# Performance work log

Hardware: AMD Instinct MI355X
Metric: run time of the kernel (lower is better)

Reference implementation:

```python
import jax, jax.numpy as jnp
import numpy as np
import math

N_HEADS = 16


def setup_inputs() -> dict:
    key = jax.random.key(0)
    ks = jax.random.split(key, 8)
    B, N, H = 4, 1024, 1024
    hidden_states = jax.random.normal(ks[0], (B, N, H), dtype=jnp.float32)
    # per-sample valid length in [N//2, N]; padding_vector is nonzero on valid
    # positions, zero afterwards (first zero index defines the pad boundary)
    lengths = jax.random.randint(ks[1], (B,), N // 2, N + 1)
    padding_vector = (jnp.arange(N)[None, :] < lengths[:, None]).astype(jnp.int32)
    s = 0.02
    Wq = jax.random.normal(ks[2], (H, H), dtype=jnp.float32) * s
    Wk = jax.random.normal(ks[3], (H, H), dtype=jnp.float32) * s
    Wv = jax.random.normal(ks[4], (H, H), dtype=jnp.float32) * s
    bq = jnp.zeros((H,), dtype=jnp.float32)
    bk = jnp.zeros((H,), dtype=jnp.float32)
    bv = jnp.zeros((H,), dtype=jnp.float32)
    return dict(hidden_states=hidden_states, padding_vector=padding_vector,
                Wq=Wq, bq=bq, Wk=Wk, bk=bk, Wv=Wv, bv=bv, max_n_codes=N)


def _heads(x, n_heads):
    B, N, H = x.shape
    return x.reshape(B, N, n_heads, H // n_heads).transpose(0, 2, 1, 3)  # (B,h,N,d)


def reference(hidden_states, padding_vector, Wq, bq, Wk, bk, Wv, bv, max_n_codes):
    B, N, H = hidden_states.shape
    d = H // N_HEADS
    q = _heads(hidden_states @ Wq.T + bq, N_HEADS)  # (B,h,N,d)
    k = _heads(hidden_states @ Wk.T + bk, N_HEADS)
    v = _heads(hidden_states @ Wv.T + bv, N_HEADS)
    scores = jnp.einsum('bhnd,bhmd->bhnm', q, k) / math.sqrt(d)
    # padd = index of first zero in padding_vector, or N if no zero
    is_zero = padding_vector == 0
    padd = jnp.where(is_zero.any(axis=1), jnp.argmax(is_zero, axis=1), N)  # (B,)
    idx = jnp.arange(N)
    valid = idx[None, :] < padd[:, None]                      # (B,N)
    keep = valid[:, None, :, None] & valid[:, None, None, :]  # (B,1,N,N)
    # masked positions get -inf pre-softmax, then are zeroed post-softmax.
    # finfo.min instead of -inf keeps fully-masked rows NaN-free; they are
    # zeroed by the post-softmax mask exactly as in the torch version.
    neg = jnp.finfo(scores.dtype).min
    probs = jax.nn.softmax(jnp.where(keep, scores, neg), axis=-1)
    probs = jnp.where(keep, probs, 0.0)
    attention_values = probs.sum(axis=-2)                     # (B,h,N)
    context = jnp.einsum('bhnm,bhmd->bhnd', probs, v)
    return (attention_values, k, q, context, scores)
```

## Files before the change

kernel.cpp:

```cpp
#include <hip/hip_runtime.h>
#include <math.h>

#define B_ 4
#define N_ 1024
#define H_ 1024
#define NH_ 16
#define D_ 64

#define SZ_ATTN (B_*NH_*N_)
#define SZ_HEADS (B_*NH_*N_*D_)

typedef __attribute__((ext_vector_type(8))) short short8v;
typedef __attribute__((ext_vector_type(4))) short short4v;
typedef __attribute__((ext_vector_type(4))) float floatx4;

__device__ inline unsigned short f2bf(float x) {
    union { float f; unsigned int u; } v; v.f = x;
    unsigned int r = v.u + 0x7FFFu + ((v.u >> 16) & 1u);
    return (unsigned short)(r >> 16);
}
__device__ inline float bf2f(unsigned short u) {
    union { unsigned int i; float f; } v; v.i = ((unsigned int)u) << 16;
    return v.f;
}

__global__ void padd_kernel(const int* __restrict__ pv, int* __restrict__ padd) {
    __shared__ int mn;
    const int b = blockIdx.x;
    if (threadIdx.x == 0) mn = N_;
    __syncthreads();
    for (int m = threadIdx.x; m < N_; m += blockDim.x)
        if (pv[b*N_ + m] == 0) atomicMin(&mn, m);
    __syncthreads();
    if (threadIdx.x == 0) padd[b] = mn;
}

__global__ __launch_bounds__(256)
void proj3_mfma_kernel(const float* __restrict__ X,
                       const float* __restrict__ Wq, const float* __restrict__ bq_, float* __restrict__ Oq,
                       const float* __restrict__ Wk, const float* __restrict__ bk_, float* __restrict__ Ok,
                       const float* __restrict__ Wv, const float* __restrict__ bv_, float* __restrict__ Ov)
{
    const int which = blockIdx.z;
    const float* __restrict__ W    = (which == 0) ? Wq  : (which == 1) ? Wk  : Wv;
    const float* __restrict__ bias = (which == 0) ? bq_ : (which == 1) ? bk_ : bv_;
    float* __restrict__ outH       = (which == 0) ? Oq  : (which == 1) ? Ok  : Ov;

    __shared__ __align__(16) unsigned short Abf[128*64];
    __shared__ __align__(16) unsigned short Bbf[128*64];

    const int tid  = threadIdx.x;
    const int lane = tid & 63;
    const int w    = tid >> 6;
    const int wr   = w >> 1, wc = w & 1;
    const int fr   = lane & 15, hi = lane >> 4;
    const int i0 = blockIdx.y * 128;
    const int j0 = blockIdx.x * 128;

    floatx4 acc[4][4];
    #pragma unroll
    for (int mi = 0; mi < 4; ++mi)
        #pragma unroll
        for (int ni = 0; ni < 4; ++ni)
            acc[mi][ni] = (floatx4){0.f, 0.f, 0.f, 0.f};

    for (int kt = 0; kt < H_; kt += 64) {
        __syncthreads();
        #pragma unroll
        for (int l = 0; l < 4; ++l) {
            const int e = tid + 256*l;
            const int row = e >> 3, kc = e & 7;
            const int sw = ((kc ^ (row & 7)) << 3);
            {
                const float* src = X + (size_t)(i0+row)*H_ + kt + kc*8;
                const float4 xa = *(const float4*)(src);
                const float4 xb = *(const float4*)(src + 4);
                short8v pk;
                pk[0] = (short)f2bf(xa.x); pk[1] = (short)f2bf(xa.y);
                pk[2] = (short)f2bf(xa.z); pk[3] = (short)f2bf(xa.w);
                pk[4] = (short)f2bf(xb.x); pk[5] = (short)f2bf(xb.y);
                pk[6] = (short)f2bf(xb.z); pk[7] = (short)f2bf(xb.w);
                *(short8v*)&Abf[row*64 + sw] = pk;
            }
            {
                const float* src = W + (size_t)(j0+row)*H_ + kt + kc*8;
                const float4 wa = *(const float4*)(src);
                const float4 wb = *(const float4*)(src + 4);
                short8v pk;
                pk[0] = (short)f2bf(wa.x); pk[1] = (short)f2bf(wa.y);
                pk[2] = (short)f2bf(wa.z); pk[3] = (short)f2bf(wa.w);
                pk[4] = (short)f2bf(wb.x); pk[5] = (short)f2bf(wb.y);
                pk[6] = (short)f2bf(wb.z); pk[7] = (short)f2bf(wb.w);
                *(short8v*)&Bbf[row*64 + sw] = pk;
            }
        }
        __syncthreads();

        #pragma unroll
        for (int ks = 0; ks < 2; ++ks) {
            short8v a[4], b[4];
            #pragma unroll
            for (int mi = 0; mi < 4; ++mi) {
                const int row = wr*64 + mi*16 + fr;
                a[mi] = *(const short8v*)&Abf[row*64 + (((ks*4 + hi) ^ (fr & 7)) << 3)];
            }
            #pragma unroll
            for (int ni = 0; ni < 4; ++ni) {
                const int row = wc*64 + ni*16 + fr;
                b[ni] = *(const short8v*)&Bbf[row*64 + (((ks*4 + hi) ^ (fr & 7)) << 3)];
            }
            #pragma unroll
            for (int mi = 0; mi < 4; ++mi)
                #pragma unroll
                for (int ni = 0; ni < 4; ++ni)
                    acc[mi][ni] = __builtin_amdgcn_mfma_f32_16x16x32_bf16(
                        a[mi], b[ni], acc[mi][ni], 0, 0, 0);
        }
    }

    #pragma unroll
    for (int ni = 0; ni < 4; ++ni) {
        const int j = j0 + wc*64 + ni*16 + fr;
        const int head = j >> 6, d = j & 63;
        const float bvj = bias[j];
        #pragma unroll
        for (int mi = 0; mi < 4; ++mi) {
            #pragma unroll
            for (int reg = 0; reg < 4; ++reg) {
                const int i = i0 + wr*64 + mi*16 + hi*4 + reg;
                const int bb = i >> 10, n = i & 1023;
                outH[((size_t)(bb*NH_ + head)*N_ + n)*D_ + d] = acc[mi][ni][reg] + bvj;
            }
        }
    }
}

__global__ __launch_bounds__(256)
void fused_attn_mfma(const float* __restrict__ Q, const float* __restrict__ K,
                     const float* __restrict__ Vh, const int* __restrict__ padd,
                     float* __restrict__ S, float* __restrict__ ctx,
                     float* __restrict__ attn)
{
    __shared__ __align__(16) unsigned short Abf[128*64];
    __shared__ __align__(16) unsigned short Bbf[64*64];
    __shared__ float smx[128], sinv[128];
    __shared__ float cred[256];

    const int tid  = threadIdx.x;
    const int lane = tid & 63;
    const int w    = tid >> 6;
    const int fr   = lane & 15, hi = lane >> 4;
    const int bh = blockIdx.y;
    const int n0 = blockIdx.x * 128;
    const int b  = bh >> 4;
    const int pd = padd[b];
    const float* Qb = Q  + (size_t)bh*N_*D_;
    const float* Kb = K  + (size_t)bh*N_*D_;
    const float* Vb = Vh + (size_t)bh*N_*D_;
    float* Sb = S + (size_t)bh*N_*N_;

    #pragma unroll
    for (int l = 0; l < 4; ++l) {
        const int e = tid + 256*l;
        const int row = e >> 3, kc = e & 7;
        const float* src = Qb + (size_t)(n0+row)*D_ + kc*8;
        const float4 xa = *(const float4*)(src);
        const float4 xb = *(const float4*)(src + 4);
        short8v pk;
        pk[0] = (short)f2bf(xa.x); pk[1] = (short)f2bf(xa.y);
        pk[2] = (short)f2bf(xa.z); pk[3] = (short)f2bf(xa.w);
        pk[4] = (short)f2bf(xb.x); pk[5] = (short)f2bf(xb.y);
        pk[6] = (short)f2bf(xb.z); pk[7] = (short)f2bf(xb.w);
        *(short8v*)&Abf[row*64 + ((kc ^ (row & 7)) << 3)] = pk;
    }
    __syncthreads();

    short8v qa[2][2];
    #pragma unroll
    for (int mi = 0; mi < 2; ++mi)
        #pragma unroll
        for (int ks = 0; ks < 2; ++ks) {
            const int arow = w*32 + mi*16 + fr;
            qa[mi][ks] = *(const short8v*)&Abf[arow*64 + (((ks*4 + hi) ^ (fr & 7)) << 3)];
        }

    float run_mx[2][4], run_sm[2][4];
    #pragma unroll
    for (int mi = 0; mi < 2; ++mi)
        #pragma unroll
        for (int reg = 0; reg < 4; ++reg) { run_mx[mi][reg] = -INFINITY; run_sm[mi][reg] = 0.f; }

    for (int m0 = 0; m0 < N_; m0 += 64) {
        #pragma unroll
        for (int l = 0; l < 2; ++l) {
            const int e = tid + 256*l;
            const int row = e >> 3, kc = e & 7;
            const float* src = Kb + (size_t)(m0+row)*D_ + kc*8;
            const float4 xa = *(const float4*)(src);
            const float4 xb = *(const float4*)(src + 4);
            short8v pk;
            pk[0] = (short)f2bf(xa.x); pk[1] = (short)f2bf(xa.y);
            pk[2] = (short)f2bf(xa.z); pk[3] = (short)f2bf(xa.w);
            pk[4] = (short)f2bf(xb.x); pk[5] = (short)f2bf(xb.y);
            pk[6] = (short)f2bf(xb.z); pk[7] = (short)f2bf(xb.w);
            *(short8v*)&Bbf[row*64 + ((kc ^ (row & 7)) << 3)] = pk;
        }
        __syncthreads();

        floatx4 sacc[2][4];
        #pragma unroll
        for (int mi = 0; mi < 2; ++mi)
            #pragma unroll
            for (int ni = 0; ni < 4; ++ni)
                sacc[mi][ni] = (floatx4){0.f, 0.f, 0.f, 0.f};

        #pragma unroll
        for (int ks = 0; ks < 2; ++ks) {
            short8v kb[4];
            #pragma unroll
            for (int ni = 0; ni < 4; ++ni) {
                const int brow = ni*16 + fr;
                kb[ni] = *(const short8v*)&Bbf[brow*64 + (((ks*4 + hi) ^ (fr & 7)) << 3)];
            }
            #pragma unroll
            for (int mi = 0; mi < 2; ++mi)
                #pragma unroll
                for (int ni = 0; ni < 4; ++ni)
                    sacc[mi][ni] = __builtin_amdgcn_mfma_f32_16x16x32_bf16(
                        qa[mi][ks], kb[ni], sacc[mi][ni], 0, 0, 0);
        }

        #pragma unroll
        for (int mi = 0; mi < 2; ++mi)
            #pragma unroll
            for (int ni = 0; ni < 4; ++ni) {
                sacc[mi][ni] *= 0.125f;
                const int m = m0 + ni*16 + fr;
                #pragma unroll
                for (int reg = 0; reg < 4; ++reg) {
                    const int n = n0 + w*32 + mi*16 + hi*4 + reg;
                    Sb[(size_t)n*N_ + m] = sacc[mi][ni][reg];
                }
            }

        if (m0 < pd) {
            #pragma unroll
            for (int mi = 0; mi < 2; ++mi)
                #pragma unroll
                for (int reg = 0; reg < 4; ++reg) {
                    float tm = -INFINITY;
                    #pragma unroll
                    for (int ni = 0; ni < 4; ++ni)
                        if (m0 + ni*16 + fr < pd) tm = fmaxf(tm, sacc[mi][ni][reg]);
                    tm = fmaxf(tm, __shfl_xor(tm, 1, 64));
                    tm = fmaxf(tm, __shfl_xor(tm, 2, 64));
                    tm = fmaxf(tm, __shfl_xor(tm, 4, 64));
                    tm = fmaxf(tm, __shfl_xor(tm, 8, 64));
                    const float nm = fmaxf(run_mx[mi][reg], tm);
                    float s = 0.f;
                    #pragma unroll
                    for (int ni = 0; ni < 4; ++ni)
                        if (m0 + ni*16 + fr < pd) s += __expf(sacc[mi][ni][reg] - nm);
                    s += __shfl_xor(s, 1, 64);
                    s += __shfl_xor(s, 2, 64);
                    s += __shfl_xor(s, 4, 64);
                    s += __shfl_xor(s, 8, 64);
                    run_sm[mi][reg] = run_sm[mi][reg]*__expf(run_mx[mi][reg] - nm) + s;
                    run_mx[mi][reg] = nm;
                }
        }
        __syncthreads();
    }

    if (n0 >= pd) {
        #pragma unroll
        for (int l = 0; l < 8; ++l) {
            const int e = tid + 256*l;
            const int row = e >> 4, c4 = e & 15;
            float4 z; z.x = z.y = z.z = z.w = 0.f;
            *(float4*)(ctx + ((size_t)bh*N_ + n0 + row)*D_ + c4*4) = z;
        }
        return;
    }

    if (fr == 0) {
        #pragma unroll
        for (int mi = 0; mi < 2; ++mi)
            #pragma unroll
            for (int reg = 0; reg < 4; ++reg) {
                const int row = w*32 + mi*16 + hi*4 + reg;
                const bool v = (n0 + row) < pd;
                smx[row]  = v ? run_mx[mi][reg] : 0.f;
                sinv[row] = v ? 1.f/run_sm[mi][reg] : 0.f;
            }
    }
    __syncthreads();

    floatx4 acc2[2][4];
    #pragma unroll
    for (int mi = 0; mi < 2; ++mi)
        #pragma unroll
        for (int ni = 0; ni < 4; ++ni)
            acc2[mi][ni] = (floatx4){0.f, 0.f, 0.f, 0.f};

    for (int m0 = 0; m0 < pd; m0 += 64) {
        #pragma unroll
        for (int l = 0; l < 8; ++l) {
            const int e = tid + 256*l;
            const int row = e >> 4, c4 = e & 15;
            const int n = n0 + row;
            const int m = m0 + c4*4;
            const float4 s4 = *(const float4*)(Sb + (size_t)n*N_ + m);
            const bool rv = n < pd;
            const float fmx = smx[row], fiv = sinv[row];
            short4v pk;
            pk[0] = (short)f2bf((rv && m+0 < pd) ? __expf(s4.x - fmx)*fiv : 0.f);
            pk[1] = (short)f2bf((rv && m+1 < pd) ? __expf(s4.y - fmx)*fiv : 0.f);
            pk[2] = (short)f2bf((rv && m+2 < pd) ? __expf(s4.z - fmx)*fiv : 0.f);
            pk[3] = (short)f2bf((rv && m+3 < pd) ? __expf(s4.w - fmx)*fiv : 0.f);
            const int elem = row*64 + (((c4 >> 1) ^ (row & 7)) << 3) + (c4 & 1)*4;
            *(short4v*)&Abf[elem] = pk;
        }
        {
            const int d = tid & 63, mg = tid >> 6;
            #pragma unroll
            for (int jj = 0; jj < 2; ++jj) {
                short8v pk;
                #pragma unroll
                for (int j = 0; j < 8; ++j)
                    pk[j] = (short)f2bf(Vb[(size_t)(m0 + mg*16 + jj*8 + j)*D_ + d]);
                const int chunk = mg*2 + jj;
                *(short8v*)&Bbf[d*64 + ((chunk ^ (d & 7)) << 3)] = pk;
            }
        }
        __syncthreads();

        {
            const int ml = tid & 63, q = tid >> 6;
            float cs = 0.f;
            #pragma unroll
            for (int i = 0; i < 32; ++i) {
                const int row = q*32 + i;
                cs += bf2f(Abf[row*64 + (((ml >> 3) ^ (row & 7)) << 3) + (ml & 7)]);
            }
            cred[tid] = cs;
        }
        __syncthreads();
        if (tid < 64) {
            const float vtot = cred[tid] + cred[tid+64] + cred[tid+128] + cred[tid+192];
            atomicAdd(&attn[(size_t)bh*N_ + m0 + tid], vtot);
        }

        #pragma unroll
        for (int ks = 0; ks < 2; ++ks) {
            short8v a[2], vfr[4];
            #pragma unroll
            for (int mi = 0; mi < 2; ++mi) {
                const int arow = w*32 + mi*16 + fr;
                a[mi] = *(const short8v*)&Abf[arow*64 + (((ks*4 + hi) ^ (fr & 7)) << 3)];
            }
            #pragma unroll
            for (int ni = 0; ni < 4; ++ni) {
                const int bd = ni*16 + fr;
                vfr[ni] = *(const short8v*)&Bbf[bd*64 + (((ks*4 + hi) ^ (fr & 7)) << 3)];
            }
            #pragma unroll
            for (int mi = 0; mi < 2; ++mi)
                #pragma unroll
                for (int ni = 0; ni < 4; ++ni)
                    acc2[mi][ni] = __builtin_amdgcn_mfma_f32_16x16x32_bf16(
                        a[mi], vfr[ni], acc2[mi][ni], 0, 0, 0);
        }
        __syncthreads();
    }

    #pragma unroll
    for (int mi = 0; mi < 2; ++mi)
        #pragma unroll
        for (int ni = 0; ni < 4; ++ni) {
            const int d = ni*16 + fr;
            #pragma unroll
            for (int reg = 0; reg < 4; ++reg) {
                const int n = n0 + w*32 + mi*16 + hi*4 + reg;
                ctx[((size_t)bh*N_ + n)*D_ + d] = acc2[mi][ni][reg];
            }
        }
}

extern "C" void kernel_launch(void* const* d_in, const int* in_sizes, int n_in,
                              void* d_out, int out_size, void* d_ws, size_t ws_size,
                              hipStream_t stream)
{
    const float* hs = (const float*)d_in[0];
    const int*   pv = (const int*)d_in[1];
    const float* Wq = (const float*)d_in[2];
    const float* bq = (const float*)d_in[3];
    const float* Wk = (const float*)d_in[4];
    const float* bk = (const float*)d_in[5];
    const float* Wv = (const float*)d_in[6];
    const float* bv = (const float*)d_in[7];
    float* out = (float*)d_out;

    float* out_attn = out;
    float* out_k    = out_attn + SZ_ATTN;
    float* out_q    = out_k + SZ_HEADS;
    float* out_ctx  = out_q + SZ_HEADS;
    float* out_sc   = out_ctx + SZ_HEADS;

    int*   padd = (int*)d_ws;
    float* v_ws = (float*)((char*)d_ws + 256);

    hipMemsetAsync(out_attn, 0, SZ_ATTN*sizeof(float), stream);
    padd_kernel<<<B_, 256, 0, stream>>>(pv, padd);

    dim3 pg(H_/128, (B_*N_)/128, 3);
    proj3_mfma_kernel<<<pg, 256, 0, stream>>>(hs, Wq, bq, out_q,
                                              Wk, bk, out_k,
                                              Wv, bv, v_ws);

    dim3 fg(N_/128, B_*NH_);
    fused_attn_mfma<<<fg, 256, 0, stream>>>(out_q, out_k, v_ws, padd,
                                            out_sc, out_ctx, out_attn);
}
```

Measured before the change: 536.2 us.

## Pre-convert X and weights to swizzled bf16 tiles, load via global_load_lds

Adds a conversion kernel that turns X and the three weight matrices into bf16 once, stored in a tile-contiguous, pre-swizzled layout inside the scores output buffer, which serves as scratch. The projection GEMM then fills shared memory with direct global-to-LDS 16-byte loads instead of loading fp32 and converting in every block. This removes the repeated fp32 reads and conversions, since each X tile was previously converted by 24 blocks, and halves the bytes the GEMM reads. The cost is an extra kernel launch plus a round trip of the bf16 copy through memory. It relies on the attention kernel overwriting the scores buffer later.

```diff
diff --git a/kernel.cpp b/kernel.cpp
--- a/kernel.cpp
+++ b/kernel.cpp
@@ -10,9 +10,19 @@
 #define SZ_ATTN (B_*NH_*N_)
 #define SZ_HEADS (B_*NH_*N_*D_)
 
+#define XT_CHUNKS (32*16*1024)
+#define WT_CHUNKS (8*16*1024)
+
 typedef __attribute__((ext_vector_type(8))) short short8v;
 typedef __attribute__((ext_vector_type(4))) short short4v;
 typedef __attribute__((ext_vector_type(4))) float floatx4;
+
+typedef __attribute__((address_space(1))) const unsigned int gau32;
+typedef __attribute__((address_space(3))) unsigned int lau32;
+
+__device__ inline void gl16(const unsigned short* g, unsigned short* l) {
+    __builtin_amdgcn_global_load_lds((gau32*)g, (lau32*)l, 16, 0, 0);
+}
 
 __device__ inline unsigned short f2bf(float x) {
     union { float f; unsigned int u; } v; v.f = x;
@@ -36,13 +46,47 @@
 }
 
 __global__ __launch_bounds__(256)
-void proj3_mfma_kernel(const float* __restrict__ X,
-                       const float* __restrict__ Wq, const float* __restrict__ bq_, float* __restrict__ Oq,
-                       const float* __restrict__ Wk, const float* __restrict__ bk_, float* __restrict__ Ok,
-                       const float* __restrict__ Wv, const float* __restrict__ bv_, float* __restrict__ Ov)
+void convert_kernel(const float* __restrict__ X,  const float* __restrict__ Wq,
+                    const float* __restrict__ Wk, const float* __restrict__ Wv,
+                    unsigned short* __restrict__ scratch)
+{
+    const int g = blockIdx.x*256 + threadIdx.x;
+    const float* src;
+    if (g < XT_CHUNKS) {
+        const int c = g & 1023, t = g >> 10;
+        const int it = t >> 4, kt = t & 15;
+        const int row = c >> 3, kcs = c & 7, kc = kcs ^ (row & 7);
+        src = X + (size_t)(it*128 + row)*H_ + kt*64 + kc*8;
+    } else {
+        const int gw = g - XT_CHUNKS;
+        const int which = gw >> 17;
+        const int rem = gw & (WT_CHUNKS-1);
+        const int c = rem & 1023, t = rem >> 10;
+        const int jt = t >> 4, kt = t & 15;
+        const int row = c >> 3, kcs = c & 7, kc = kcs ^ (row & 7);
+        const float* W = (which == 0) ? Wq : (which == 1) ? Wk : Wv;
+        src = W + (size_t)(jt*128 + row)*H_ + kt*64 + kc*8;
+    }
+    const float4 a = *(const float4*)src;
+    const float4 b = *(const float4*)(src + 4);
+    short8v pk;
+    pk[0] = (short)f2bf(a.x); pk[1] = (short)f2bf(a.y);
+    pk[2] = (short)f2bf(a.z); pk[3] = (short)f2bf(a.w);
+    pk[4] = (short)f2bf(b.x); pk[5] = (short)f2bf(b.y);
+    pk[6] = (short)f2bf(b.z); pk[7] = (short)f2bf(b.w);
+    *(short8v*)(scratch + (size_t)g*8) = pk;
+}
+
+__global__ __launch_bounds__(256)
+void proj3_mfma_kernel(const unsigned short* __restrict__ Xt,
+                       const unsigned short* __restrict__ Wt_all,
+                       const float* __restrict__ bq_, const float* __restrict__ bk_,
+                       const float* __restrict__ bv_,
+                       float* __restrict__ Oq, float* __restrict__ Ok,
+                       float* __restrict__ Ov)
 {
     const int which = blockIdx.z;
-    const float* __restrict__ W    = (which == 0) ? Wq  : (which == 1) ? Wk  : Wv;
+    const unsigned short* __restrict__ Wt = Wt_all + (size_t)which*WT_CHUNKS*8;
     const float* __restrict__ bias = (which == 0) ? bq_ : (which == 1) ? bk_ : bv_;
     float* __restrict__ outH       = (which == 0) ? Oq  : (which == 1) ? Ok  : Ov;
 
@@ -64,35 +108,15 @@
         for (int ni = 0; ni < 4; ++ni)
             acc[mi][ni] = (floatx4){0.f, 0.f, 0.f, 0.f};
 
-    for (int kt = 0; kt < H_; kt += 64) {
-        __syncthreads();
+    for (int ktile = 0; ktile < 16; ++ktile) {
+        __syncthreads();
+        const unsigned short* xsrc = Xt + (size_t)(blockIdx.y*16 + ktile)*8192;
+        const unsigned short* wsrc = Wt + (size_t)(blockIdx.x*16 + ktile)*8192;
         #pragma unroll
         for (int l = 0; l < 4; ++l) {
-            const int e = tid + 256*l;
-            const int row = e >> 3, kc = e & 7;
-            const int sw = ((kc ^ (row & 7)) << 3);
-            {
-                const float* src = X + (size_t)(i0+row)*H_ + kt + kc*8;
-                const float4 xa = *(const float4*)(src);
-                const float4 xb = *(const float4*)(src + 4);
-                short8v pk;
-                pk[0] = (short)f2bf(xa.x); pk[1] = (short)f2bf(xa.y);
-                pk[2] = (short)f2bf(xa.z); pk[3] = (short)f2bf(xa.w);
-                pk[4] = (short)f2bf(xb.x); pk[5] = (short)f2bf(xb.y);
-                pk[6] = (short)f2bf(xb.z); pk[7] = (short)f2bf(xb.w);
-                *(short8v*)&Abf[row*64 + sw] = pk;
-            }
-            {
-                const float* src = W + (size_t)(j0+row)*H_ + kt + kc*8;
-                const float4 wa = *(const float4*)(src);
-                const float4 wb = *(const float4*)(src + 4);
-                short8v pk;
-                pk[0] = (short)f2bf(wa.x); pk[1] = (short)f2bf(wa.y);
-                pk[2] = (short)f2bf(wa.z); pk[3] = (short)f2bf(wa.w);
-                pk[4] = (short)f2bf(wb.x); pk[5] = (short)f2bf(wb.y);
-                pk[6] = (short)f2bf(wb.z); pk[7] = (short)f2bf(wb.w);
-                *(short8v*)&Bbf[row*64 + sw] = pk;
-            }
+            const int ch = l*256 + tid;
+            gl16(xsrc + (size_t)ch*8, Abf + (size_t)ch*8);
+            gl16(wsrc + (size_t)ch*8, Bbf + (size_t)ch*8);
         }
         __syncthreads();
 
@@ -410,13 +434,19 @@
     int*   padd = (int*)d_ws;
     float* v_ws = (float*)((char*)d_ws + 256);
 
+    unsigned short* scratch = (unsigned short*)out_sc;
+    const unsigned short* Xt = scratch;
+    const unsigned short* Wt = scratch + (size_t)XT_CHUNKS*8;
+
     hipMemsetAsync(out_attn, 0, SZ_ATTN*sizeof(float), stream);
     padd_kernel<<<B_, 256, 0, stream>>>(pv, padd);
 
+    convert_kernel<<<(XT_CHUNKS + 3*WT_CHUNKS)/256, 256, 0, stream>>>(
+        hs, Wq, Wk, Wv, scratch);
+
     dim3 pg(H_/128, (B_*N_)/128, 3);
-    proj3_mfma_kernel<<<pg, 256, 0, stream>>>(hs, Wq, bq, out_q,
-                                              Wk, bk, out_k,
-                                              Wv, bv, v_ws);
+    proj3_mfma_kernel<<<pg, 256, 0, stream>>>(Xt, Wt, bq, bk, bv,
+                                              out_q, out_k, v_ws);
 
     dim3 fg(N_/128, B_*NH_);
     fused_attn_mfma<<<fg, 256, 0, stream>>>(out_q, out_k, v_ws, padd,
```

New measurement: 492.4 us. 8.2% less time.
